# Kernel tuning notes

Hardware: AMD Instinct MI355X
Metric: run time of the kernel (lower is better)

The kernel has to match this reference:

```python
import jax, jax.numpy as jnp
from jax import lax
import numpy as np

VGG_C = 512
INNER = 32


def _conv3x3(x, w, b):
    # x: [B,C,H,W], w: [O,I,3,3], padding=1 (SAME)
    y = lax.conv_general_dilated(x, w, (1, 1), 'SAME',
                                 dimension_numbers=('NCHW', 'OIHW', 'NCHW'))
    return y + b[None, :, None, None]


def _predict_filter(style, cw, cb, fw, fb):
    # FilterPredictor_S: conv 512->32, global mean pool, FC 32 -> 9*32*32
    s = _conv3x3(style, cw, cb)                     # [B,32,H,W]
    pooled = s.mean(axis=(2, 3))                    # [B,32]
    f = pooled @ fw.T + fb                          # [B,9216]
    return f.reshape(-1, INNER, INNER, 3, 3)        # [B,outC,inC,3,3]


def _apply_filter(x, filt):
    # per-sample dynamic 3x3 conv: x [B,32,H,W], filt [B,32,32,3,3]
    def one(xi, wi):
        return lax.conv_general_dilated(xi[None], wi, (1, 1), 'SAME',
                                        dimension_numbers=('NCHW', 'OIHW', 'NCHW'))[0]
    return jax.vmap(one)(x, filt)


def setup_inputs() -> dict:
    key = jax.random.key(0)
    ks = jax.random.split(key, 16)
    B, H, W = 8, 64, 64
    sc = 0.02
    d = {
        'content': jax.random.normal(ks[0], (B, VGG_C, H, W), jnp.float32),
        'style': jax.random.normal(ks[1], (B, VGG_C, H, W), jnp.float32),
        'ds_w': jax.random.normal(ks[2], (INNER, VGG_C, 3, 3), jnp.float32) * sc,
        'ds_b': jnp.zeros((INNER,), jnp.float32),
        'up_w': jax.random.normal(ks[3], (VGG_C, INNER, 3, 3), jnp.float32) * sc,
        'up_b': jnp.zeros((VGG_C,), jnp.float32),
        'f1_cw': jax.random.normal(ks[4], (INNER, VGG_C, 3, 3), jnp.float32) * sc,
        'f1_cb': jnp.zeros((INNER,), jnp.float32),
        'f1_fw': jax.random.normal(ks[5], (9 * INNER * INNER, INNER), jnp.float32) * sc,
        'f1_fb': jnp.zeros((9 * INNER * INNER,), jnp.float32),
        'f2_cw': jax.random.normal(ks[6], (INNER, VGG_C, 3, 3), jnp.float32) * sc,
        'f2_cb': jnp.zeros((INNER,), jnp.float32),
        'f2_fw': jax.random.normal(ks[7], (9 * INNER * INNER, INNER), jnp.float32) * sc,
        'f2_fb': jnp.zeros((9 * INNER * INNER,), jnp.float32),
    }
    return d


def reference(content, style, ds_w, ds_b, up_w, up_b,
              f1_cw, f1_cb, f1_fw, f1_fb,
              f2_cw, f2_cb, f2_fw, f2_fb):
    c = _conv3x3(content, ds_w, ds_b)                       # [B,32,H,W]
    filt1 = _predict_filter(style, f1_cw, f1_cb, f1_fw, f1_fb)
    c = _apply_filter(c, filt1)
    c = jnp.where(c >= 0, c, 0.2 * c)                       # LeakyReLU(0.2)
    filt2 = _predict_filter(style, f2_cw, f2_cb, f2_fw, f2_fb)
    c = _apply_filter(c, filt2)
    return content + _conv3x3(c, up_w, up_b)
```

## Files before the change

kernel.cpp:

```cpp
#include <hip/hip_runtime.h>
#include <hip/hip_bf16.h>

#define NB 8
#define NC 512
#define HW 4096
#define INNER 32

typedef unsigned short u16;
typedef unsigned int u32;
typedef __attribute__((ext_vector_type(8))) short bf16x8;
typedef __attribute__((ext_vector_type(4))) float f32x4;

__device__ __forceinline__ float b2f(u16 u) {
    union { u32 a; float f; } z;
    z.a = ((u32)u) << 16;
    return z.f;
}

__device__ __forceinline__ u16 f2b(float v) {
    u32 x = __float_as_uint(v);
    return (u16)((x + 0x7fffu + ((x >> 16) & 1u)) >> 16);
}

__device__ __forceinline__ float ldin(const void* p, int idx, int isf32) {
    if (isf32) return ((const float*)p)[idx];
    return b2f(((const u16*)p)[idx]);
}

__device__ __forceinline__ void gld_lds16(const void* g, void* l) {
    __builtin_amdgcn_global_load_lds(
        (const __attribute__((address_space(1))) unsigned int*)g,
        (__attribute__((address_space(3))) unsigned int*)l, 16, 0, 0);
}

__global__ __launch_bounds__(256) void k_detect(const u16* __restrict__ content,
                                                int* __restrict__ flag) {
    __shared__ int scnt;
    if (threadIdx.x == 0) scnt = 0;
    __syncthreads();
    u16 u = content[threadIdx.x * 2048];
    int e = (u >> 7) & 0xff;
    if (e >= 100 && e <= 150) atomicAdd(&scnt, 1);
    __syncthreads();
    if (threadIdx.x == 0) *flag = (scnt < 128) ? 1 : 0;
}

__global__ __launch_bounds__(256) void k_prep_wdown(const void* __restrict__ dsw,
        u16* __restrict__ Bp, const int* __restrict__ flag) {
    int isf32 = *flag;
    int idx = blockIdx.x * 256 + threadIdx.x;
    int e = idx & 7, l = (idx >> 3) & 63, nf = (idx >> 9) & 1;
    int cb = (idx >> 10) & 15, t9 = idx >> 14;
    int oc = nf * 16 + (l & 15);
    int c = cb * 32 + (l >> 4) * 8 + e;
    Bp[idx] = f2b(ldin(dsw, (oc * NC + c) * 9 + t9, isf32));
}

__global__ __launch_bounds__(256) void k_prep_wup(const void* __restrict__ upw,
        u16* __restrict__ B2p, const int* __restrict__ flag) {
    int isf32 = *flag;
    int idx = blockIdx.x * 256 + threadIdx.x;
    int e = idx & 7, l = (idx >> 3) & 63, nfo = (idx >> 9) & 31, t9 = idx >> 14;
    int oc = nfo * 16 + (l & 15);
    int ic = (l >> 4) * 8 + e;
    B2p[idx] = f2b(ldin(upw, (oc * INNER + ic) * 9 + t9, isf32));
}

__global__ __launch_bounds__(256) void k_transform(const void* __restrict__ content,
        u16* __restrict__ cT, int bstart, const int* __restrict__ flag) {
    int isf32 = *flag;
    int h  = blockIdx.x & 63;
    int ci = (blockIdx.x >> 6) & 15;
    int b4 = blockIdx.x >> 10;
    int tid = threadIdx.x;
    __shared__ float lds[32 * 65];
    size_t gbase = ((size_t)(bstart + b4) * NC + ci * 32) * HW + (size_t)h * 64;
    if (isf32) {
#pragma unroll
        for (int k = 0; k < 2; k++) {
            int q = tid + k * 256;
            int c = q >> 4, w0 = (q & 15) * 4;
            float4 v = *(const float4*)((const float*)content + gbase + (size_t)c * HW + w0);
            lds[c * 65 + w0 + 0] = v.x;
            lds[c * 65 + w0 + 1] = v.y;
            lds[c * 65 + w0 + 2] = v.z;
            lds[c * 65 + w0 + 3] = v.w;
        }
    } else {
        int c = tid >> 3, w0 = (tid & 7) * 8;
        uint4 v = *(const uint4*)((const u16*)content + gbase + (size_t)c * HW + w0);
        lds[c * 65 + w0 + 0] = b2f((u16)(v.x & 0xffffu));
        lds[c * 65 + w0 + 1] = b2f((u16)(v.x >> 16));
        lds[c * 65 + w0 + 2] = b2f((u16)(v.y & 0xffffu));
        lds[c * 65 + w0 + 3] = b2f((u16)(v.y >> 16));
        lds[c * 65 + w0 + 4] = b2f((u16)(v.z & 0xffffu));
        lds[c * 65 + w0 + 5] = b2f((u16)(v.z >> 16));
        lds[c * 65 + w0 + 6] = b2f((u16)(v.w & 0xffffu));
        lds[c * 65 + w0 + 7] = b2f((u16)(v.w >> 16));
    }
    __syncthreads();
    u32* out = (u32*)(cT + ((size_t)(b4 * 16 + ci) * 4096 + h * 64) * 32);
#pragma unroll
    for (int k = 0; k < 4; k++) {
        int j = tid + k * 256;
        int w = j >> 4, cpair = j & 15;
        int key = (w + 1) & 3;
        int p0 = cpair << 1;
        int lc = (((p0 >> 3) ^ key) << 3) | (p0 & 7);
        u32 v = (u32)f2b(lds[lc * 65 + w]) | ((u32)f2b(lds[(lc + 1) * 65 + w]) << 16);
        out[j] = v;
    }
}

__global__ __launch_bounds__(256) void k_style_stats(const void* __restrict__ style,
        float* __restrict__ S, const int* __restrict__ flag) {
    int isf32 = *flag;
    int bc = blockIdx.x;
    int base = bc * HW;
    int tid = threadIdx.x;
    float t = 0.f, top = 0.f, bot = 0.f, lft = 0.f, rgt = 0.f;
    for (int e = tid; e < HW; e += 256) {
        float v = ldin(style, base + e, isf32);
        int h = e >> 6, w = e & 63;
        t += v;
        top += (h == 0)  ? v : 0.f;
        bot += (h == 63) ? v : 0.f;
        lft += (w == 0)  ? v : 0.f;
        rgt += (w == 63) ? v : 0.f;
    }
#pragma unroll
    for (int off = 32; off > 0; off >>= 1) {
        t   += __shfl_down(t, off);
        top += __shfl_down(top, off);
        bot += __shfl_down(bot, off);
        lft += __shfl_down(lft, off);
        rgt += __shfl_down(rgt, off);
    }
    __shared__ float red[4][5];
    int wave = tid >> 6;
    if ((tid & 63) == 0) {
        red[wave][0] = t; red[wave][1] = top; red[wave][2] = bot;
        red[wave][3] = lft; red[wave][4] = rgt;
    }
    __syncthreads();
    if (tid == 0) {
        t   = red[0][0] + red[1][0] + red[2][0] + red[3][0];
        top = red[0][1] + red[1][1] + red[2][1] + red[3][1];
        bot = red[0][2] + red[1][2] + red[2][2] + red[3][2];
        lft = red[0][3] + red[1][3] + red[2][3] + red[3][3];
        rgt = red[0][4] + red[1][4] + red[2][4] + red[3][4];
        float c00 = ldin(style, base + 0,    isf32);
        float c0W = ldin(style, base + 63,   isf32);
        float cH0 = ldin(style, base + 4032, isf32);
        float cHW = ldin(style, base + 4095, isf32);
        float* o = S + bc * 9;
        o[0] = t - bot - rgt + cHW;
        o[1] = t - bot;
        o[2] = t - bot - lft + cH0;
        o[3] = t - rgt;
        o[4] = t;
        o[5] = t - lft;
        o[6] = t - top - rgt + c0W;
        o[7] = t - top;
        o[8] = t - top - lft + c00;
    }
}

__global__ __launch_bounds__(64) void k_pooled(const float* __restrict__ S,
        const void* __restrict__ cw1, const void* __restrict__ cb1,
        const void* __restrict__ cw2, const void* __restrict__ cb2,
        float* __restrict__ pooled, const int* __restrict__ flag) {
    int isf32 = *flag;
    int set = blockIdx.y;
    int b = blockIdx.x >> 5;
    int o = blockIdx.x & 31;
    const void* cw = set ? cw2 : cw1;
    const void* cb = set ? cb2 : cb1;
    int lane = threadIdx.x;
    float acc = 0.f;
    const float* Sb = S + b * NC * 9;
    int wbase = o * NC * 9;
    for (int c = lane; c < NC; c += 64) {
#pragma unroll
        for (int k = 0; k < 9; k++)
            acc += Sb[c * 9 + k] * ldin(cw, wbase + c * 9 + k, isf32);
    }
#pragma unroll
    for (int off = 32; off > 0; off >>= 1) acc += __shfl_down(acc, off);
    if (lane == 0)
        pooled[(set * NB + b) * INNER + o] = acc * (1.0f / 4096.0f) + ldin(cb, o, isf32);
}

__global__ __launch_bounds__(256) void k_fc(const float* __restrict__ pooled,
        const void* __restrict__ fw1, const void* __restrict__ fb1,
        const void* __restrict__ fw2, const void* __restrict__ fb2,
        u16* __restrict__ fpack, const int* __restrict__ flag) {
    int isf32 = *flag;
    int set = blockIdx.y;
    int b = blockIdx.x / 36;
    int chunk = blockIdx.x - b * 36;
    int row = chunk * 256 + threadIdx.x;
    const void* fw = set ? fw2 : fw1;
    const void* fb = set ? fb2 : fb1;
    __shared__ float p[32];
    if (threadIdx.x < 32) p[threadIdx.x] = pooled[(set * NB + b) * 32 + threadIdx.x];
    __syncthreads();
    float acc = ldin(fb, row, isf32);
    if (isf32) {
        const float* fwf = (const float*)fw + row * 32;
#pragma unroll
        for (int j = 0; j < 32; j++) acc += fwf[j] * p[j];
    } else {
        const u32* w32 = (const u32*)((const u16*)fw + row * 32);
#pragma unroll
        for (int j = 0; j < 16; j++) {
            u32 u = w32[j];
            acc += b2f((u16)(u & 0xffffu)) * p[2 * j];
            acc += b2f((u16)(u >> 16)) * p[2 * j + 1];
        }
    }
    int oc = row / 288;
    int rem = row - oc * 288;
    int ic = rem / 9;
    int t9 = rem - ic * 9;
    int l = (oc & 15) | ((ic >> 3) << 4);
    int e = ic & 7;
    int nf = oc >> 4;
    fpack[((((set * NB + b) * 9 + t9) * 2 + nf) * 64 + l) * 8 + e] = f2b(acc);
}

__global__ __launch_bounds__(256) void k_conv_down(const u16* __restrict__ cT,
        const u16* __restrict__ Bp, const void* __restrict__ dsb,
        u16* __restrict__ c0T, int bstart, const int* __restrict__ flag) {
    int isf32 = *flag;
    int b4 = blockIdx.x >> 6, row = blockIdx.x & 63;
    int b = bstart + b4;
    int tid = threadIdx.x, lane = tid & 63;
    int wid = __builtin_amdgcn_readfirstlane(tid >> 6);
    __shared__ u16 lds[3 * 66 * 32];
    u32* lds32 = (u32*)lds;
    for (int i = tid; i < 3 * 66 * 16; i += 256) lds32[i] = 0u;
    __syncthreads();

    int m = lane & 15, g = lane >> 4;
    int wbase = wid * 16;
    int j = wid * 64 + lane;
    f32x4 acc0 = {0.f, 0.f, 0.f, 0.f}, acc1 = {0.f, 0.f, 0.f, 0.f};

    for (int ci = 0; ci < 16; ci++) {
        if (ci) __syncthreads();
        const u16* sp = cT + ((size_t)(b4 * 16 + ci) * 4096) * 32;
#pragma unroll
        for (int r = 0; r < 3; r++) {
            int gh = row + r - 1;
            if (gh >= 0 && gh < 64)
                gld_lds16(sp + (size_t)gh * 2048 + j * 8,
                          (char*)lds + (r * 66 + 1) * 64 + wid * 1024);
        }
        __syncthreads();
#pragma unroll
        for (int t9 = 0; t9 < 9; t9++) {
            int dh = t9 / 3, dw = t9 - dh * 3;
            int wi = wbase + m + dw;
            bf16x8 a = *(const bf16x8*)(lds + ((dh * 66 + wi) * 32 + (g ^ (wi & 3)) * 8));
            bf16x8 b0 = ((const bf16x8*)Bp)[((t9 * 16 + ci) * 2 + 0) * 64 + lane];
            bf16x8 b1 = ((const bf16x8*)Bp)[((t9 * 16 + ci) * 2 + 1) * 64 + lane];
            acc0 = __builtin_amdgcn_mfma_f32_16x16x32_bf16(a, b0, acc0, 0, 0, 0);
            acc1 = __builtin_amdgcn_mfma_f32_16x16x32_bf16(a, b1, acc1, 0, 0, 0);
        }
    }
    float bia0 = ldin(dsb, m, isf32);
    float bia1 = ldin(dsb, 16 + m, isf32);
    size_t obase = ((size_t)b * 4096 + row * 64) * 32;
    int pix0 = wbase + g * 4;
#pragma unroll
    for (int r = 0; r < 4; r++) {
        int w = pix0 + r;
        int key = (w + 1) & 3;
        int p0 = (((m >> 3) ^ key) << 3) | (m & 7);
        int p1 = ((((16 + m) >> 3) ^ key) << 3) | (m & 7);
        c0T[obase + (size_t)w * 32 + p0] = f2b(acc0[r] + bia0);
        c0T[obase + (size_t)w * 32 + p1] = f2b(acc1[r] + bia1);
    }
}

__global__ __launch_bounds__(256) void k_apply(const u16* __restrict__ srcT,
        const u16* __restrict__ fpack, u16* __restrict__ dstT, int lrelu) {
    int b = blockIdx.x >> 6, row = blockIdx.x & 63;
    int tid = threadIdx.x, lane = tid & 63;
    int wid = __builtin_amdgcn_readfirstlane(tid >> 6);
    __shared__ u16 lds[3 * 66 * 32];
    u32* lds32 = (u32*)lds;
    for (int i = tid; i < 96; i += 256) {
        int r = i >> 5, side = (i >> 4) & 1, cpr = i & 15;
        lds32[(r * 66 + side * 65) * 16 + cpr] = 0u;
    }
    const u16* sp = srcT + (size_t)b * 64 * 64 * 32;
    for (int r = 0; r < 3; r++) {
        int gh = row + r - 1;
        u32 ldsoff = (u32)(r * 66 + 1) * 64 + (u32)wid * 1024;
        if (gh >= 0 && gh < 64) {
            int j = wid * 64 + lane;
            gld_lds16(sp + (size_t)gh * 2048 + j * 8, (char*)lds + ldsoff);
        } else {
            int4 z = make_int4(0, 0, 0, 0);
            *(int4*)((char*)lds + ldsoff + (u32)lane * 16) = z;
        }
    }
    __syncthreads();

    int m = lane & 15, g = lane >> 4, wbase = wid * 16;
    f32x4 acc0 = {0.f, 0.f, 0.f, 0.f}, acc1 = {0.f, 0.f, 0.f, 0.f};
    const bf16x8* FB = (const bf16x8*)fpack + (size_t)b * 1152;
#pragma unroll
    for (int t9 = 0; t9 < 9; t9++) {
        int dh = t9 / 3, dw = t9 - dh * 3;
        int wi = wbase + m + dw;
        bf16x8 a = *(const bf16x8*)(lds + ((dh * 66 + wi) * 32 + (g ^ (wi & 3)) * 8));
        bf16x8 b0 = FB[(t9 * 2 + 0) * 64 + lane];
        bf16x8 b1 = FB[(t9 * 2 + 1) * 64 + lane];
        acc0 = __builtin_amdgcn_mfma_f32_16x16x32_bf16(a, b0, acc0, 0, 0, 0);
        acc1 = __builtin_amdgcn_mfma_f32_16x16x32_bf16(a, b1, acc1, 0, 0, 0);
    }
    size_t obase = ((size_t)(b * 64 + row) * 64) * 32;
    int pix0 = wbase + g * 4;
#pragma unroll
    for (int r = 0; r < 4; r++) {
        float v0 = acc0[r], v1 = acc1[r];
        if (lrelu) {
            v0 = (v0 >= 0.f) ? v0 : 0.2f * v0;
            v1 = (v1 >= 0.f) ? v1 : 0.2f * v1;
        }
        int w = pix0 + r;
        int key = (w + 1) & 3;
        int p0 = (((m >> 3) ^ key) << 3) | (m & 7);
        int p1 = ((((16 + m) >> 3) ^ key) << 3) | (m & 7);
        dstT[obase + (size_t)w * 32 + p0] = f2b(v0);
        dstT[obase + (size_t)w * 32 + p1] = f2b(v1);
    }
}

__global__ __launch_bounds__(256) void k_conv_up(const u16* __restrict__ c2T,
        const u16* __restrict__ B2p, const void* __restrict__ upb,
        const void* __restrict__ content, void* __restrict__ outv,
        const int* __restrict__ flag) {
    int isf32 = *flag;
    int b = blockIdx.x >> 6, row = blockIdx.x & 63;
    int nq = blockIdx.y;
    int tid = threadIdx.x, lane = tid & 63;
    int wid = __builtin_amdgcn_readfirstlane(tid >> 6);
    __shared__ u16 lds[3 * 66 * 32];
    u32* lds32 = (u32*)lds;
    for (int i = tid; i < 96; i += 256) {
        int r = i >> 5, side = (i >> 4) & 1, cpr = i & 15;
        lds32[(r * 66 + side * 65) * 16 + cpr] = 0u;
    }
    const u16* sp = c2T + (size_t)b * 64 * 64 * 32;
    for (int r = 0; r < 3; r++) {
        int gh = row + r - 1;
        u32 ldsoff = (u32)(r * 66 + 1) * 64 + (u32)wid * 1024;
        if (gh >= 0 && gh < 64) {
            int j = wid * 64 + lane;
            gld_lds16(sp + (size_t)gh * 2048 + j * 8, (char*)lds + ldsoff);
        } else {
            int4 z = make_int4(0, 0, 0, 0);
            *(int4*)((char*)lds + ldsoff + (u32)lane * 16) = z;
        }
    }
    __syncthreads();

    int m = lane & 15, g = lane >> 4, wbase = wid * 16;
    f32x4 acc[8];
#pragma unroll
    for (int i = 0; i < 8; i++) acc[i] = (f32x4){0.f, 0.f, 0.f, 0.f};
#pragma unroll
    for (int t9 = 0; t9 < 9; t9++) {
        int dh = t9 / 3, dw = t9 - dh * 3;
        int wi = wbase + m + dw;
        bf16x8 a = *(const bf16x8*)(lds + ((dh * 66 + wi) * 32 + (g ^ (wi & 3)) * 8));
#pragma unroll
        for (int nfl = 0; nfl < 8; nfl++) {
            bf16x8 bw = ((const bf16x8*)B2p)[(t9 * 32 + nq * 8 + nfl) * 64 + lane];
            acc[nfl] = __builtin_amdgcn_mfma_f32_16x16x32_bf16(a, bw, acc[nfl], 0, 0, 0);
        }
    }
    int pix0 = wbase + g * 4;
#pragma unroll
    for (int nfl = 0; nfl < 8; nfl++) {
        int oc = nq * 128 + nfl * 16 + m;
        size_t idx = ((size_t)b * NC + oc) * HW + (size_t)row * 64 + pix0;
        float bias = ldin(upb, oc, isf32);
        if (isf32) {
            f32x4 rsd = *(const f32x4*)((const float*)content + idx);
            f32x4 v;
#pragma unroll
            for (int r = 0; r < 4; r++) v[r] = acc[nfl][r] + bias + rsd[r];
            *(f32x4*)((float*)outv + idx) = v;
        } else {
#pragma unroll
            for (int r = 0; r < 4; r++) {
                float rv = b2f(((const u16*)content)[idx + r]);
                ((u16*)outv)[idx + r] = f2b(acc[nfl][r] + bias + rv);
            }
        }
    }
}

extern "C" void kernel_launch(void* const* d_in, const int* in_sizes, int n_in,
                              void* d_out, int out_size, void* d_ws, size_t ws_size,
                              hipStream_t stream) {
    const void* content = d_in[0];
    const void* style   = d_in[1];
    const void* ds_w    = d_in[2];
    const void* ds_b    = d_in[3];
    const void* up_w    = d_in[4];
    const void* up_b    = d_in[5];
    const void* f1_cw   = d_in[6];
    const void* f1_cb   = d_in[7];
    const void* f1_fw   = d_in[8];
    const void* f1_fb   = d_in[9];
    const void* f2_cw   = d_in[10];
    const void* f2_cb   = d_in[11];
    const void* f2_fw   = d_in[12];
    const void* f2_fb   = d_in[13];

    float* S      = (float*)d_out;
    float* pooled = S + 36864;
    u16*   fpack  = (u16*)(pooled + 512);
    u16*   Bpack  = fpack + 147456;
    u16*   c0T    = Bpack + 147456;
    u16*   c1T    = c0T + 1048576;
    u16*   cTh    = c1T + 1048576;

    int*   flag   = (int*)d_ws;
    u16*   B2pack = (u16*)((char*)d_ws + 16);
    u16*   c2T    = B2pack + 147456;

    k_detect<<<1, 256, 0, stream>>>((const u16*)content, flag);
    k_prep_wdown<<<576, 256, 0, stream>>>(ds_w, Bpack, flag);
    k_prep_wup<<<576, 256, 0, stream>>>(up_w, B2pack, flag);
    k_style_stats<<<NB * NC, 256, 0, stream>>>(style, S, flag);
    k_pooled<<<dim3(NB * 32, 2), 64, 0, stream>>>(S, f1_cw, f1_cb, f2_cw, f2_cb, pooled, flag);
    k_fc<<<dim3(NB * 36, 2), 256, 0, stream>>>(pooled, f1_fw, f1_fb, f2_fw, f2_fb, fpack, flag);
    for (int half = 0; half < 2; half++) {
        int bstart = half * 4;
        k_transform<<<4 * 16 * 64, 256, 0, stream>>>(content, cTh, bstart, flag);
        k_conv_down<<<4 * 64, 256, 0, stream>>>(cTh, Bpack, ds_b, c0T, bstart, flag);
    }
    k_apply<<<NB * 64, 256, 0, stream>>>(c0T, fpack, c1T, 1);
    k_apply<<<NB * 64, 256, 0, stream>>>(c1T, fpack + NB * 9216, c2T, 0);
    k_conv_up<<<dim3(NB * 64, 4), 256, 0, stream>>>(c2T, B2pack, up_b, content, d_out, flag);
}
```

Before: 330.9 us.

## Merge prep stages into multi-role kernels and stage conv_up epilogue through LDS

Folds the detect, weight-pack, style-stats, transform, pooled and fc kernels into two multi-role launches (k_front/k_mid) that dispatch on block index. This cuts launch count and lets independent stages run concurrently. The dtype flag is now taken from the host input size or a per-wave ballot instead of a separate detect kernel. When workspace is large enough, all 8 batches are transformed in one pass using d_out as scratch. The conv_up epilogue is staged through LDS so residual loads and output stores are coalesced and vectorized, including the bf16 path.

```diff
diff --git a/kernel.cpp b/kernel.cpp
--- a/kernel.cpp
+++ b/kernel.cpp
@@ -33,89 +33,18 @@
         (__attribute__((address_space(3))) unsigned int*)l, 16, 0, 0);
 }
 
-__global__ __launch_bounds__(256) void k_detect(const u16* __restrict__ content,
-                                                int* __restrict__ flag) {
-    __shared__ int scnt;
-    if (threadIdx.x == 0) scnt = 0;
-    __syncthreads();
-    u16 u = content[threadIdx.x * 2048];
+__device__ __forceinline__ int resolve_isf32(int hisf, const void* content) {
+    if (hisf >= 0) return hisf;
+    int lane = threadIdx.x & 63;
+    u16 u = ((const u16*)content)[lane * 2048];
     int e = (u >> 7) & 0xff;
-    if (e >= 100 && e <= 150) atomicAdd(&scnt, 1);
-    __syncthreads();
-    if (threadIdx.x == 0) *flag = (scnt < 128) ? 1 : 0;
-}
-
-__global__ __launch_bounds__(256) void k_prep_wdown(const void* __restrict__ dsw,
-        u16* __restrict__ Bp, const int* __restrict__ flag) {
-    int isf32 = *flag;
-    int idx = blockIdx.x * 256 + threadIdx.x;
-    int e = idx & 7, l = (idx >> 3) & 63, nf = (idx >> 9) & 1;
-    int cb = (idx >> 10) & 15, t9 = idx >> 14;
-    int oc = nf * 16 + (l & 15);
-    int c = cb * 32 + (l >> 4) * 8 + e;
-    Bp[idx] = f2b(ldin(dsw, (oc * NC + c) * 9 + t9, isf32));
-}
-
-__global__ __launch_bounds__(256) void k_prep_wup(const void* __restrict__ upw,
-        u16* __restrict__ B2p, const int* __restrict__ flag) {
-    int isf32 = *flag;
-    int idx = blockIdx.x * 256 + threadIdx.x;
-    int e = idx & 7, l = (idx >> 3) & 63, nfo = (idx >> 9) & 31, t9 = idx >> 14;
-    int oc = nfo * 16 + (l & 15);
-    int ic = (l >> 4) * 8 + e;
-    B2p[idx] = f2b(ldin(upw, (oc * INNER + ic) * 9 + t9, isf32));
-}
-
-__global__ __launch_bounds__(256) void k_transform(const void* __restrict__ content,
-        u16* __restrict__ cT, int bstart, const int* __restrict__ flag) {
-    int isf32 = *flag;
-    int h  = blockIdx.x & 63;
-    int ci = (blockIdx.x >> 6) & 15;
-    int b4 = blockIdx.x >> 10;
-    int tid = threadIdx.x;
-    __shared__ float lds[32 * 65];
-    size_t gbase = ((size_t)(bstart + b4) * NC + ci * 32) * HW + (size_t)h * 64;
-    if (isf32) {
-#pragma unroll
-        for (int k = 0; k < 2; k++) {
-            int q = tid + k * 256;
-            int c = q >> 4, w0 = (q & 15) * 4;
-            float4 v = *(const float4*)((const float*)content + gbase + (size_t)c * HW + w0);
-            lds[c * 65 + w0 + 0] = v.x;
-            lds[c * 65 + w0 + 1] = v.y;
-            lds[c * 65 + w0 + 2] = v.z;
-            lds[c * 65 + w0 + 3] = v.w;
-        }
-    } else {
-        int c = tid >> 3, w0 = (tid & 7) * 8;
-        uint4 v = *(const uint4*)((const u16*)content + gbase + (size_t)c * HW + w0);
-        lds[c * 65 + w0 + 0] = b2f((u16)(v.x & 0xffffu));
-        lds[c * 65 + w0 + 1] = b2f((u16)(v.x >> 16));
-        lds[c * 65 + w0 + 2] = b2f((u16)(v.y & 0xffffu));
-        lds[c * 65 + w0 + 3] = b2f((u16)(v.y >> 16));
-        lds[c * 65 + w0 + 4] = b2f((u16)(v.z & 0xffffu));
-        lds[c * 65 + w0 + 5] = b2f((u16)(v.z >> 16));
-        lds[c * 65 + w0 + 6] = b2f((u16)(v.w & 0xffffu));
-        lds[c * 65 + w0 + 7] = b2f((u16)(v.w >> 16));
-    }
-    __syncthreads();
-    u32* out = (u32*)(cT + ((size_t)(b4 * 16 + ci) * 4096 + h * 64) * 32);
-#pragma unroll
-    for (int k = 0; k < 4; k++) {
-        int j = tid + k * 256;
-        int w = j >> 4, cpair = j & 15;
-        int key = (w + 1) & 3;
-        int p0 = cpair << 1;
-        int lc = (((p0 >> 3) ^ key) << 3) | (p0 & 7);
-        u32 v = (u32)f2b(lds[lc * 65 + w]) | ((u32)f2b(lds[(lc + 1) * 65 + w]) << 16);
-        out[j] = v;
-    }
-}
-
-__global__ __launch_bounds__(256) void k_style_stats(const void* __restrict__ style,
-        float* __restrict__ S, const int* __restrict__ flag) {
-    int isf32 = *flag;
-    int bc = blockIdx.x;
+    unsigned long long m = __ballot(e >= 100 && e <= 150);
+    return (__popcll(m) < 32) ? 1 : 0;
+}
+
+
+__device__ __forceinline__ void role_style(int bc, const void* style, float* S,
+                                           int isf32, float* smf) {
     int base = bc * HW;
     int tid = threadIdx.x;
     float t = 0.f, top = 0.f, bot = 0.f, lft = 0.f, rgt = 0.f;
@@ -136,19 +65,18 @@
         lft += __shfl_down(lft, off);
         rgt += __shfl_down(rgt, off);
     }
-    __shared__ float red[4][5];
     int wave = tid >> 6;
     if ((tid & 63) == 0) {
-        red[wave][0] = t; red[wave][1] = top; red[wave][2] = bot;
-        red[wave][3] = lft; red[wave][4] = rgt;
+        smf[wave * 5 + 0] = t; smf[wave * 5 + 1] = top; smf[wave * 5 + 2] = bot;
+        smf[wave * 5 + 3] = lft; smf[wave * 5 + 4] = rgt;
     }
     __syncthreads();
     if (tid == 0) {
-        t   = red[0][0] + red[1][0] + red[2][0] + red[3][0];
-        top = red[0][1] + red[1][1] + red[2][1] + red[3][1];
-        bot = red[0][2] + red[1][2] + red[2][2] + red[3][2];
-        lft = red[0][3] + red[1][3] + red[2][3] + red[3][3];
-        rgt = red[0][4] + red[1][4] + red[2][4] + red[3][4];
+        t   = smf[0] + smf[5] + smf[10] + smf[15];
+        top = smf[1] + smf[6] + smf[11] + smf[16];
+        bot = smf[2] + smf[7] + smf[12] + smf[17];
+        lft = smf[3] + smf[8] + smf[13] + smf[18];
+        rgt = smf[4] + smf[9] + smf[14] + smf[19];
         float c00 = ldin(style, base + 0,    isf32);
         float c0W = ldin(style, base + 63,   isf32);
         float cH0 = ldin(style, base + 4032, isf32);
@@ -166,43 +94,79 @@
     }
 }
 
-__global__ __launch_bounds__(64) void k_pooled(const float* __restrict__ S,
-        const void* __restrict__ cw1, const void* __restrict__ cb1,
-        const void* __restrict__ cw2, const void* __restrict__ cb2,
-        float* __restrict__ pooled, const int* __restrict__ flag) {
-    int isf32 = *flag;
-    int set = blockIdx.y;
-    int b = blockIdx.x >> 5;
-    int o = blockIdx.x & 31;
-    const void* cw = set ? cw2 : cw1;
-    const void* cb = set ? cb2 : cb1;
-    int lane = threadIdx.x;
-    float acc = 0.f;
-    const float* Sb = S + b * NC * 9;
-    int wbase = o * NC * 9;
-    for (int c = lane; c < NC; c += 64) {
-#pragma unroll
-        for (int k = 0; k < 9; k++)
-            acc += Sb[c * 9 + k] * ldin(cw, wbase + c * 9 + k, isf32);
-    }
-#pragma unroll
-    for (int off = 32; off > 0; off >>= 1) acc += __shfl_down(acc, off);
-    if (lane == 0)
-        pooled[(set * NB + b) * INNER + o] = acc * (1.0f / 4096.0f) + ldin(cb, o, isf32);
-}
-
-__global__ __launch_bounds__(256) void k_fc(const float* __restrict__ pooled,
-        const void* __restrict__ fw1, const void* __restrict__ fb1,
-        const void* __restrict__ fw2, const void* __restrict__ fb2,
-        u16* __restrict__ fpack, const int* __restrict__ flag) {
-    int isf32 = *flag;
-    int set = blockIdx.y;
-    int b = blockIdx.x / 36;
-    int chunk = blockIdx.x - b * 36;
+__device__ __forceinline__ void role_transform(int ridx, const void* content,
+        u16* cT, int bstart, int isf32, float* lds) {
+    int h  = ridx & 63;
+    int ci = (ridx >> 6) & 15;
+    int b4 = ridx >> 10;
+    int tid = threadIdx.x;
+    size_t gbase = ((size_t)(bstart + b4) * NC + ci * 32) * HW + (size_t)h * 64;
+    if (isf32) {
+#pragma unroll
+        for (int k = 0; k < 2; k++) {
+            int q = tid + k * 256;
+            int c = q >> 4, w0 = (q & 15) * 4;
+            float4 v = *(const float4*)((const float*)content + gbase + (size_t)c * HW + w0);
+            lds[c * 65 + w0 + 0] = v.x;
+            lds[c * 65 + w0 + 1] = v.y;
+            lds[c * 65 + w0 + 2] = v.z;
+            lds[c * 65 + w0 + 3] = v.w;
+        }
+    } else {
+        int c = tid >> 3, w0 = (tid & 7) * 8;
+        uint4 v = *(const uint4*)((const u16*)content + gbase + (size_t)c * HW + w0);
+        lds[c * 65 + w0 + 0] = b2f((u16)(v.x & 0xffffu));
+        lds[c * 65 + w0 + 1] = b2f((u16)(v.x >> 16));
+        lds[c * 65 + w0 + 2] = b2f((u16)(v.y & 0xffffu));
+        lds[c * 65 + w0 + 3] = b2f((u16)(v.y >> 16));
+        lds[c * 65 + w0 + 4] = b2f((u16)(v.z & 0xffffu));
+        lds[c * 65 + w0 + 5] = b2f((u16)(v.z >> 16));
+        lds[c * 65 + w0 + 6] = b2f((u16)(v.w & 0xffffu));
+        lds[c * 65 + w0 + 7] = b2f((u16)(v.w >> 16));
+    }
+    __syncthreads();
+    u32* out = (u32*)(cT + ((size_t)(b4 * 16 + ci) * 4096 + h * 64) * 32);
+#pragma unroll
+    for (int k = 0; k < 4; k++) {
+        int j = tid + k * 256;
+        int w = j >> 4, cpair = j & 15;
+        int key = (w + 1) & 3;
+        int p0 = cpair << 1;
+        int lc = (((p0 >> 3) ^ key) << 3) | (p0 & 7);
+        u32 v = (u32)f2b(lds[lc * 65 + w]) | ((u32)f2b(lds[(lc + 1) * 65 + w]) << 16);
+        out[j] = v;
+    }
+}
+
+__device__ __forceinline__ void role_prep_wdown(int ridx, const void* dsw,
+        u16* Bp, int isf32) {
+    int idx = ridx * 256 + threadIdx.x;
+    int e = idx & 7, l = (idx >> 3) & 63, nf = (idx >> 9) & 1;
+    int cb = (idx >> 10) & 15, t9 = idx >> 14;
+    int oc = nf * 16 + (l & 15);
+    int c = cb * 32 + (l >> 4) * 8 + e;
+    Bp[idx] = f2b(ldin(dsw, (oc * NC + c) * 9 + t9, isf32));
+}
+
+__device__ __forceinline__ void role_prep_wup(int ridx, const void* upw,
+        u16* B2p, int isf32) {
+    int idx = ridx * 256 + threadIdx.x;
+    int e = idx & 7, l = (idx >> 3) & 63, nfo = (idx >> 9) & 31, t9 = idx >> 14;
+    int oc = nfo * 16 + (l & 15);
+    int ic = (l >> 4) * 8 + e;
+    B2p[idx] = f2b(ldin(upw, (oc * INNER + ic) * 9 + t9, isf32));
+}
+
+__device__ __forceinline__ void role_fc(int ridx, const float* pooled,
+        const void* fw1, const void* fb1, const void* fw2, const void* fb2,
+        u16* fpack, int isf32, float* p) {
+    int set = ridx / 288;
+    int rr = ridx - set * 288;
+    int b = rr / 36;
+    int chunk = rr - b * 36;
     int row = chunk * 256 + threadIdx.x;
     const void* fw = set ? fw2 : fw1;
     const void* fb = set ? fb2 : fb1;
-    __shared__ float p[32];
     if (threadIdx.x < 32) p[threadIdx.x] = pooled[(set * NB + b) * 32 + threadIdx.x];
     __syncthreads();
     float acc = ldin(fb, row, isf32);
@@ -229,22 +193,19 @@
     fpack[((((set * NB + b) * 9 + t9) * 2 + nf) * 64 + l) * 8 + e] = f2b(acc);
 }
 
-__global__ __launch_bounds__(256) void k_conv_down(const u16* __restrict__ cT,
-        const u16* __restrict__ Bp, const void* __restrict__ dsb,
-        u16* __restrict__ c0T, int bstart, const int* __restrict__ flag) {
-    int isf32 = *flag;
-    int b4 = blockIdx.x >> 6, row = blockIdx.x & 63;
+__device__ __forceinline__ void role_conv_down(int x, const u16* cT,
+        const u16* Bp, const void* dsb, u16* c0T, int bstart, int isf32,
+        u16* lds) {
+    u32* lds32 = (u32*)lds;
+    int b4 = x >> 6, row = x & 63;
     int b = bstart + b4;
     int tid = threadIdx.x, lane = tid & 63;
     int wid = __builtin_amdgcn_readfirstlane(tid >> 6);
-    __shared__ u16 lds[3 * 66 * 32];
-    u32* lds32 = (u32*)lds;
     for (int i = tid; i < 3 * 66 * 16; i += 256) lds32[i] = 0u;
     __syncthreads();
 
     int m = lane & 15, g = lane >> 4;
     int wbase = wid * 16;
-    int j = wid * 64 + lane;
     f32x4 acc0 = {0.f, 0.f, 0.f, 0.f}, acc1 = {0.f, 0.f, 0.f, 0.f};
 
     for (int ci = 0; ci < 16; ci++) {
@@ -254,7 +215,7 @@
         for (int r = 0; r < 3; r++) {
             int gh = row + r - 1;
             if (gh >= 0 && gh < 64)
-                gld_lds16(sp + (size_t)gh * 2048 + j * 8,
+                gld_lds16(sp + (size_t)gh * 2048 + tid * 8,
                           (char*)lds + (r * 66 + 1) * 64 + wid * 1024);
         }
         __syncthreads();
@@ -262,7 +223,7 @@
         for (int t9 = 0; t9 < 9; t9++) {
             int dh = t9 / 3, dw = t9 - dh * 3;
             int wi = wbase + m + dw;
-            bf16x8 a = *(const bf16x8*)(lds + ((dh * 66 + wi) * 32 + (g ^ (wi & 3)) * 8));
+            bf16x8 a = *(const bf16x8*)(lds + ((dh * 66 + wi) * 32 + ((g ^ (wi & 3)) * 8)));
             bf16x8 b0 = ((const bf16x8*)Bp)[((t9 * 16 + ci) * 2 + 0) * 64 + lane];
             bf16x8 b1 = ((const bf16x8*)Bp)[((t9 * 16 + ci) * 2 + 1) * 64 + lane];
             acc0 = __builtin_amdgcn_mfma_f32_16x16x32_bf16(a, b0, acc0, 0, 0, 0);
@@ -282,6 +243,70 @@
         c0T[obase + (size_t)w * 32 + p0] = f2b(acc0[r] + bia0);
         c0T[obase + (size_t)w * 32 + p1] = f2b(acc1[r] + bia1);
     }
+}
+
+__device__ __forceinline__ void role_pooled(int p, const float* S,
+        const void* cw1, const void* cb1, const void* cw2, const void* cb2,
+        float* pooled, int isf32) {
+    int tid = threadIdx.x;
+    int pair = p * 4 + (tid >> 6);
+    int set = pair >> 8;
+    int rem = pair & 255;
+    int b = rem >> 5;
+    int o = rem & 31;
+    const void* cw = set ? cw2 : cw1;
+    const void* cb = set ? cb2 : cb1;
+    int lane = tid & 63;
+    float acc = 0.f;
+    const float* Sb = S + b * NC * 9;
+    int wbase = o * NC * 9;
+    for (int c = lane; c < NC; c += 64) {
+#pragma unroll
+        for (int k = 0; k < 9; k++)
+            acc += Sb[c * 9 + k] * ldin(cw, wbase + c * 9 + k, isf32);
+    }
+#pragma unroll
+    for (int off = 32; off > 0; off >>= 1) acc += __shfl_down(acc, off);
+    if (lane == 0)
+        pooled[(set * NB + b) * INNER + o] = acc * (1.0f / 4096.0f) + ldin(cb, o, isf32);
+}
+
+
+__global__ __launch_bounds__(256) void k_front(
+        const void* __restrict__ style, float* __restrict__ S, int nStyle,
+        const void* __restrict__ content, u16* __restrict__ cT, int bstart, int nT,
+        const void* __restrict__ dsw, u16* __restrict__ Bp,
+        const void* __restrict__ upw, u16* __restrict__ B2p, int nPrep,
+        const float* __restrict__ pooled,
+        const void* __restrict__ fw1, const void* __restrict__ fb1,
+        const void* __restrict__ fw2, const void* __restrict__ fb2,
+        u16* __restrict__ fpack, int hisf) {
+    __shared__ float smf[32 * 65];
+    int isf32 = resolve_isf32(hisf, content);
+    int x = blockIdx.x;
+    if (x < nStyle) { role_style(x, style, S, isf32, smf); return; }
+    x -= nStyle;
+    if (x < nT) { role_transform(x, content, cT, bstart, isf32, smf); return; }
+    x -= nT;
+    if (x < nPrep) { role_prep_wdown(x, dsw, Bp, isf32); return; }
+    x -= nPrep;
+    if (x < nPrep) { role_prep_wup(x, upw, B2p, isf32); return; }
+    x -= nPrep;
+    role_fc(x, pooled, fw1, fb1, fw2, fb2, fpack, isf32, smf);
+}
+
+__global__ __launch_bounds__(256) void k_mid(
+        const u16* __restrict__ cT, const u16* __restrict__ Bp,
+        const void* __restrict__ dsb, u16* __restrict__ c0T, int bstart, int nCD,
+        const float* __restrict__ S,
+        const void* __restrict__ cw1, const void* __restrict__ cb1,
+        const void* __restrict__ cw2, const void* __restrict__ cb2,
+        float* __restrict__ pooled, const void* __restrict__ content, int hisf) {
+    __shared__ u16 lds[3 * 66 * 32];
+    int isf32 = resolve_isf32(hisf, content);
+    int x = blockIdx.x;
+    if (x < nCD) { role_conv_down(x, cT, Bp, dsb, c0T, bstart, isf32, lds); return; }
+    role_pooled(x - nCD, S, cw1, cb1, cw2, cb2, pooled, isf32);
 }
 
 __global__ __launch_bounds__(256) void k_apply(const u16* __restrict__ srcT,
@@ -300,8 +325,7 @@
         int gh = row + r - 1;
         u32 ldsoff = (u32)(r * 66 + 1) * 64 + (u32)wid * 1024;
         if (gh >= 0 && gh < 64) {
-            int j = wid * 64 + lane;
-            gld_lds16(sp + (size_t)gh * 2048 + j * 8, (char*)lds + ldsoff);
+            gld_lds16(sp + (size_t)gh * 2048 + tid * 8, (char*)lds + ldsoff);
         } else {
             int4 z = make_int4(0, 0, 0, 0);
             *(int4*)((char*)lds + ldsoff + (u32)lane * 16) = z;
@@ -316,7 +340,7 @@
     for (int t9 = 0; t9 < 9; t9++) {
         int dh = t9 / 3, dw = t9 - dh * 3;
         int wi = wbase + m + dw;
-        bf16x8 a = *(const bf16x8*)(lds + ((dh * 66 + wi) * 32 + (g ^ (wi & 3)) * 8));
+        bf16x8 a = *(const bf16x8*)(lds + ((dh * 66 + wi) * 32 + ((g ^ (wi & 3)) * 8)));
         bf16x8 b0 = FB[(t9 * 2 + 0) * 64 + lane];
         bf16x8 b1 = FB[(t9 * 2 + 1) * 64 + lane];
         acc0 = __builtin_amdgcn_mfma_f32_16x16x32_bf16(a, b0, acc0, 0, 0, 0);
@@ -342,15 +366,15 @@
 
 __global__ __launch_bounds__(256) void k_conv_up(const u16* __restrict__ c2T,
         const u16* __restrict__ B2p, const void* __restrict__ upb,
-        const void* __restrict__ content, void* __restrict__ outv,
-        const int* __restrict__ flag) {
-    int isf32 = *flag;
+        const void* __restrict__ content, void* __restrict__ outv, int hisf) {
+    int isf32 = resolve_isf32(hisf, content);
     int b = blockIdx.x >> 6, row = blockIdx.x & 63;
     int nq = blockIdx.y;
     int tid = threadIdx.x, lane = tid & 63;
     int wid = __builtin_amdgcn_readfirstlane(tid >> 6);
-    __shared__ u16 lds[3 * 66 * 32];
-    u32* lds32 = (u32*)lds;
+    __shared__ char smem[64 * 68 * 4] __attribute__((aligned(16)));
+    u16* lds = (u16*)smem;
+    u32* lds32 = (u32*)smem;
     for (int i = tid; i < 96; i += 256) {
         int r = i >> 5, side = (i >> 4) & 1, cpr = i & 15;
         lds32[(r * 66 + side * 65) * 16 + cpr] = 0u;
@@ -360,8 +384,7 @@
         int gh = row + r - 1;
         u32 ldsoff = (u32)(r * 66 + 1) * 64 + (u32)wid * 1024;
         if (gh >= 0 && gh < 64) {
-            int j = wid * 64 + lane;
-            gld_lds16(sp + (size_t)gh * 2048 + j * 8, (char*)lds + ldsoff);
+            gld_lds16(sp + (size_t)gh * 2048 + tid * 8, (char*)lds + ldsoff);
         } else {
             int4 z = make_int4(0, 0, 0, 0);
             *(int4*)((char*)lds + ldsoff + (u32)lane * 16) = z;
@@ -377,30 +400,49 @@
     for (int t9 = 0; t9 < 9; t9++) {
         int dh = t9 / 3, dw = t9 - dh * 3;
         int wi = wbase + m + dw;
-        bf16x8 a = *(const bf16x8*)(lds + ((dh * 66 + wi) * 32 + (g ^ (wi & 3)) * 8));
+        bf16x8 a = *(const bf16x8*)(lds + ((dh * 66 + wi) * 32 + ((g ^ (wi & 3)) * 8)));
 #pragma unroll
         for (int nfl = 0; nfl < 8; nfl++) {
             bf16x8 bw = ((const bf16x8*)B2p)[(t9 * 32 + nq * 8 + nfl) * 64 + lane];
             acc[nfl] = __builtin_amdgcn_mfma_f32_16x16x32_bf16(a, bw, acc[nfl], 0, 0, 0);
         }
     }
+
     int pix0 = wbase + g * 4;
-#pragma unroll
-    for (int nfl = 0; nfl < 8; nfl++) {
-        int oc = nq * 128 + nfl * 16 + m;
-        size_t idx = ((size_t)b * NC + oc) * HW + (size_t)row * 64 + pix0;
-        float bias = ldin(upb, oc, isf32);
-        if (isf32) {
-            f32x4 rsd = *(const f32x4*)((const float*)content + idx);
-            f32x4 v;
-#pragma unroll
-            for (int r = 0; r < 4; r++) v[r] = acc[nfl][r] + bias + rsd[r];
-            *(f32x4*)((float*)outv + idx) = v;
-        } else {
-#pragma unroll
-            for (int r = 0; r < 4; r++) {
-                float rv = b2f(((const u16*)content)[idx + r]);
-                ((u16*)outv)[idx + r] = f2b(acc[nfl][r] + bias + rv);
+    float* fl = (float*)smem;
+    int ocl2 = tid >> 4;
+    int px0 = (tid & 15) * 4;
+    __syncthreads();
+#pragma unroll
+    for (int hf = 0; hf < 2; hf++) {
+        if (hf) __syncthreads();
+#pragma unroll
+        for (int nf = 0; nf < 4; nf++) {
+            int ocl = nf * 16 + m;
+            *(f32x4*)(fl + ocl * 68 + pix0) = acc[hf * 4 + nf];
+        }
+        __syncthreads();
+#pragma unroll
+        for (int p = 0; p < 4; p++) {
+            int ocl = p * 16 + ocl2;
+            int oc = nq * 128 + hf * 64 + ocl;
+            float bias = ldin(upb, oc, isf32);
+            f32x4 v4 = *(const f32x4*)(fl + ocl * 68 + px0);
+            size_t idx = ((size_t)b * NC + oc) * HW + (size_t)row * 64 + px0;
+            if (isf32) {
+                f32x4 rsd = *(const f32x4*)((const float*)content + idx);
+                f32x4 ov;
+#pragma unroll
+                for (int r = 0; r < 4; r++) ov[r] = v4[r] + bias + rsd[r];
+                *(f32x4*)((float*)outv + idx) = ov;
+            } else {
+                ushort4 rv = *(const ushort4*)((const u16*)content + idx);
+                ushort4 ov;
+                ov.x = f2b(v4[0] + bias + b2f(rv.x));
+                ov.y = f2b(v4[1] + bias + b2f(rv.y));
+                ov.z = f2b(v4[2] + bias + b2f(rv.z));
+                ov.w = f2b(v4[3] + bias + b2f(rv.w));
+                *(ushort4*)((u16*)outv + idx) = ov;
             }
         }
     }
@@ -424,30 +466,71 @@
     const void* f2_fw   = d_in[12];
     const void* f2_fb   = d_in[13];
 
-    float* S      = (float*)d_out;
-    float* pooled = S + 36864;
-    u16*   fpack  = (u16*)(pooled + 512);
-    u16*   Bpack  = fpack + 147456;
-    u16*   c0T    = Bpack + 147456;
-    u16*   c1T    = c0T + 1048576;
-    u16*   cTh    = c1T + 1048576;
-
-    int*   flag   = (int*)d_ws;
-    u16*   B2pack = (u16*)((char*)d_ws + 16);
-    u16*   c2T    = B2pack + 147456;
-
-    k_detect<<<1, 256, 0, stream>>>((const u16*)content, flag);
-    k_prep_wdown<<<576, 256, 0, stream>>>(ds_w, Bpack, flag);
-    k_prep_wup<<<576, 256, 0, stream>>>(up_w, B2pack, flag);
-    k_style_stats<<<NB * NC, 256, 0, stream>>>(style, S, flag);
-    k_pooled<<<dim3(NB * 32, 2), 64, 0, stream>>>(S, f1_cw, f1_cb, f2_cw, f2_cb, pooled, flag);
-    k_fc<<<dim3(NB * 36, 2), 256, 0, stream>>>(pooled, f1_fw, f1_fb, f2_fw, f2_fb, fpack, flag);
-    for (int half = 0; half < 2; half++) {
-        int bstart = half * 4;
-        k_transform<<<4 * 16 * 64, 256, 0, stream>>>(content, cTh, bstart, flag);
-        k_conv_down<<<4 * 64, 256, 0, stream>>>(cTh, Bpack, ds_b, c0T, bstart, flag);
-    }
-    k_apply<<<NB * 64, 256, 0, stream>>>(c0T, fpack, c1T, 1);
-    k_apply<<<NB * 64, 256, 0, stream>>>(c1T, fpack + NB * 9216, c2T, 0);
-    k_conv_up<<<dim3(NB * 64, 4), 256, 0, stream>>>(c2T, B2pack, up_b, content, d_out, flag);
-}
+    int hisf = -1;
+    if (in_sizes && n_in >= 1) {
+        if (in_sizes[0] == NB * NC * HW * 4) hisf = 1;
+        else if (in_sizes[0] == NB * NC * HW * 2) hisf = 0;
+    }
+
+    const size_t SZ_PACK = 294912;
+    const size_t SZ_CT2  = 2097152;
+    const size_t REQ_WS  = 3 * SZ_CT2 + 3 * SZ_PACK + 147456 * 4 + 2048 + 64;
+
+    if (ws_size >= REQ_WS) {
+        char* w = (char*)d_ws;
+        u16*   B2pack = (u16*)w;                 w += SZ_PACK;
+        u16*   c2T    = (u16*)w;                 w += SZ_CT2;
+        u16*   c0T    = (u16*)w;                 w += SZ_CT2;
+        u16*   c1T    = (u16*)w;                 w += SZ_CT2;
+        u16*   Bpack  = (u16*)w;                 w += SZ_PACK;
+        u16*   fpack  = (u16*)w;                 w += SZ_PACK;
+        float* S      = (float*)w;               w += 147456 * 4;
+        float* pooled = (float*)w;
+        u16*   cT     = (u16*)d_out;
+
+        k_front<<<4096 + 8192 + 2 * 576, 256, 0, stream>>>(
+            style, S, 4096, content, cT, 0, 8192,
+            ds_w, Bpack, up_w, B2pack, 576,
+            pooled, f1_fw, f1_fb, f2_fw, f2_fb, fpack, hisf);
+        k_mid<<<512 + 128, 256, 0, stream>>>(
+            cT, Bpack, ds_b, c0T, 0, 512,
+            S, f1_cw, f1_cb, f2_cw, f2_cb, pooled, content, hisf);
+        k_front<<<576, 256, 0, stream>>>(
+            style, S, 0, content, cT, 0, 0,
+            ds_w, Bpack, up_w, B2pack, 0,
+            pooled, f1_fw, f1_fb, f2_fw, f2_fb, fpack, hisf);
+        k_apply<<<NB * 64, 256, 0, stream>>>(c0T, fpack, c1T, 1);
+        k_apply<<<NB * 64, 256, 0, stream>>>(c1T, fpack + NB * 9216, c2T, 0);
+        k_conv_up<<<dim3(NB * 64, 4), 256, 0, stream>>>(c2T, B2pack, up_b,
+                                                        content, d_out, hisf);
+    } else {
+        float* S      = (float*)d_out;
+        float* pooled = S + 36864;
+        u16*   fpack  = (u16*)(pooled + 512);
+        u16*   Bpack  = fpack + 147456;
+        u16*   c0T    = Bpack + 147456;
+        u16*   c1T    = c0T + 1048576;
+        u16*   cTh    = c1T + 1048576;
+        u16*   B2pack = (u16*)d_ws;
+        u16*   c2T    = B2pack + 147456;
+
+        k_front<<<4096 + 4096 + 2 * 576, 256, 0, stream>>>(
+            style, S, 4096, content, cTh, 0, 4096,
+            ds_w, Bpack, up_w, B2pack, 576,
+            pooled, f1_fw, f1_fb, f2_fw, f2_fb, fpack, hisf);
+        k_mid<<<256 + 128, 256, 0, stream>>>(
+            cTh, Bpack, ds_b, c0T, 0, 256,
+            S, f1_cw, f1_cb, f2_cw, f2_cb, pooled, content, hisf);
+        k_front<<<4096 + 576, 256, 0, stream>>>(
+            style, S, 0, content, cTh, 4, 4096,
+            ds_w, Bpack, up_w, B2pack, 0,
+            pooled, f1_fw, f1_fb, f2_fw, f2_fb, fpack, hisf);
+        k_mid<<<256, 256, 0, stream>>>(
+            cTh, Bpack, ds_b, c0T, 4, 256,
+            S, f1_cw, f1_cb, f2_cw, f2_cb, pooled, content, hisf);
+        k_apply<<<NB * 64, 256, 0, stream>>>(c0T, fpack, c1T, 1);
+        k_apply<<<NB * 64, 256, 0, stream>>>(c1T, fpack + NB * 9216, c2T, 0);
+        k_conv_up<<<dim3(NB * 64, 4), 256, 0, stream>>>(c2T, B2pack, up_b,
+                                                        content, d_out, hisf);
+    }
+}
```

New measurement: 283.6 us. 14.3% less time.
